# Kernel tuning notes

Hardware: AMD Instinct MI355X
Metric: run time of the kernel (lower is better)

The kernel has to match this reference:

```python
import jax, jax.numpy as jnp
import numpy as np

# Model hyperparameters (from init_kwargs)
D_MODEL = 1536
NUM_HEADS = 16
QUERY_GROUPS = 4
HEAD_DIM = D_MODEL // NUM_HEADS          # 96
HEADS_PER_GROUP = NUM_HEADS // QUERY_GROUPS
ROPE_THETA = 10000.0
T_GRID, H_GRID, W_GRID = 32, 16, 16      # patch_size
AXIS_DIM = HEAD_DIM // 3                 # 32 dims per RoPE axis (t, h, w)

B = 2
S = H_GRID * W_GRID                      # 256 spatial patches per frame
N = T_GRID * S


def _angles(pos, dim, theta):
    # pos: [P] int -> angles [P, dim//2]
    inv_freq = 1.0 / (theta ** (jnp.arange(0, dim, 2, dtype=jnp.float32) / dim))
    return pos.astype(jnp.float32)[:, None] * inv_freq[None, :]


def _rotate_half(x, cos, sin):
    # x: [..., d], cos/sin broadcastable to [..., d//2]; half-split rotation
    x1, x2 = jnp.split(x, 2, axis=-1)
    return jnp.concatenate([x1 * cos - x2 * sin, x2 * cos + x1 * sin], axis=-1)


def _rope3d(x, cos_t, sin_t, cos_h, sin_h, cos_w, sin_w):
    # x: [B, T, S, heads, HEAD_DIM]; apply RoPE per axis chunk (t | h | w)
    xt = _rotate_half(x[..., 0 * AXIS_DIM:1 * AXIS_DIM], cos_t, sin_t)
    xh = _rotate_half(x[..., 1 * AXIS_DIM:2 * AXIS_DIM], cos_h, sin_h)
    xw = _rotate_half(x[..., 2 * AXIS_DIM:3 * AXIS_DIM], cos_w, sin_w)
    return jnp.concatenate([xt, xh, xw], axis=-1)


def _rope_tables(T, S, dtype):
    ang_t = _angles(jnp.arange(T), AXIS_DIM, ROPE_THETA)            # [T, 16]
    pos_hw = jnp.arange(S)
    ang_h = _angles(pos_hw // W_GRID, AXIS_DIM, ROPE_THETA)          # [S, 16]
    ang_w = _angles(pos_hw % W_GRID, AXIS_DIM, ROPE_THETA)           # [S, 16]
    # broadcast shapes: t varies over frame axis, h/w over spatial axis
    cos_t = jnp.cos(ang_t).astype(dtype)[None, :, None, None, :]
    sin_t = jnp.sin(ang_t).astype(dtype)[None, :, None, None, :]
    cos_h = jnp.cos(ang_h).astype(dtype)[None, None, :, None, :]
    sin_h = jnp.sin(ang_h).astype(dtype)[None, None, :, None, :]
    cos_w = jnp.cos(ang_w).astype(dtype)[None, None, :, None, :]
    sin_w = jnp.sin(ang_w).astype(dtype)[None, None, :, None, :]
    return cos_t, sin_t, cos_h, sin_h, cos_w, sin_w


def setup_inputs() -> dict:
    key = jax.random.key(0)
    k1, k2, k3 = jax.random.split(key, 3)
    x = jax.random.normal(k1, (B, T_GRID, S, D_MODEL), dtype=jnp.float32)
    padding_mask = jnp.ones((B, N), dtype=bool)
    scale = D_MODEL ** -0.5
    qkv_out = (NUM_HEADS + 2 * QUERY_GROUPS) * HEAD_DIM  # 2304
    w_qkv = jax.random.normal(k2, (qkv_out, D_MODEL), dtype=jnp.float32) * scale
    w_o = jax.random.normal(k3, (D_MODEL, D_MODEL), dtype=jnp.float32) * scale
    return {"x": x, "padding_mask": padding_mask, "w_qkv": w_qkv, "w_o": w_o}


def reference(x, padding_mask, w_qkv, w_o):
    # Spatial attention mode (GQA SDPA fallback path, non-causal, key padding mask).
    Bx, T, Sx, D = x.shape
    qkv = jnp.einsum('btsd,ed->btse', x, w_qkv)  # fused qkv projection, no bias
    q_end = NUM_HEADS * HEAD_DIM
    k_end = q_end + QUERY_GROUPS * HEAD_DIM
    q = qkv[..., :q_end].reshape(Bx, T, Sx, NUM_HEADS, HEAD_DIM)
    k = qkv[..., q_end:k_end].reshape(Bx, T, Sx, QUERY_GROUPS, HEAD_DIM)
    v = qkv[..., k_end:].reshape(Bx, T, Sx, QUERY_GROUPS, HEAD_DIM)

    tabs = _rope_tables(T, Sx, x.dtype)
    q = _rope3d(q, *tabs)
    k = _rope3d(k, *tabs)

    # GQA: expand kv groups to num_heads
    k = jnp.repeat(k, HEADS_PER_GROUP, axis=3)
    v = jnp.repeat(v, HEADS_PER_GROUP, axis=3)

    # Spatial attention: each (b, t) frame attends over its S patches
    scale = 1.0 / np.sqrt(HEAD_DIM)
    scores = jnp.einsum('btqhd,btkhd->bthqk', q, k) * scale  # [B,T,H,S,S]
    key_mask = padding_mask.reshape(Bx, T, Sx)
    scores = jnp.where(key_mask[:, :, None, None, :], scores, jnp.asarray(-1e9, scores.dtype))
    attn = jax.nn.softmax(scores, axis=-1)
    out = jnp.einsum('bthqk,btkhd->btqhd', attn, v).reshape(Bx, T, Sx, D)
    return jnp.einsum('btsd,ed->btse', out, w_o)  # output projection
```

## Files before the change

### kernel.cpp

```cpp
#include <hip/hip_runtime.h>

typedef __bf16 bf16;
typedef __bf16 bf16x8 __attribute__((ext_vector_type(8)));
typedef float f32x4 __attribute__((ext_vector_type(4)));

#define AS1 __attribute__((address_space(1)))
#define AS3 __attribute__((address_space(3)))

__device__ __forceinline__ void gl_lds16(const bf16* g, bf16* s) {
  __builtin_amdgcn_global_load_lds((const AS1 void*)g, (AS3 void*)s, 16, 0, 0);
}

__global__ void cvt_f32_bf16(const float* __restrict__ in, bf16* __restrict__ out, long n) {
  long i = ((long)blockIdx.x * blockDim.x + threadIdx.x) * 8;
  if (i + 8 <= n) {
    float4 a = *(const float4*)(in + i);
    float4 b = *(const float4*)(in + i + 4);
    bf16x8 v;
    v[0] = (bf16)a.x; v[1] = (bf16)a.y; v[2] = (bf16)a.z; v[3] = (bf16)a.w;
    v[4] = (bf16)b.x; v[5] = (bf16)b.y; v[6] = (bf16)b.z; v[7] = (bf16)b.w;
    *(bf16x8*)(out + i) = v;
  }
}

__global__ void gemm_qkv(const bf16* __restrict__ A, const bf16* __restrict__ B,
                         bf16* __restrict__ C, bf16* __restrict__ Vt) {
  const int K = 1536;
  __shared__ __align__(16) bf16 As[128 * 32];
  __shared__ __align__(16) bf16 Bs[128 * 32];
  const int tid = threadIdx.x;
  const int wave = tid >> 6, lane = tid & 63;
  const int l16 = lane & 15, krow = lane >> 4;
  const int wm = (wave >> 1) * 64, wn = (wave & 1) * 64;
  const int bm = blockIdx.x, bn = blockIdx.y;
  const bf16* a_base = A + (long)bm * 128 * K;
  const bf16* b_base = B + (long)bn * 128 * K;

  f32x4 acc[4][4];
#pragma unroll
  for (int i = 0; i < 4; ++i)
#pragma unroll
    for (int j = 0; j < 4; ++j) {
      f32x4 z = {0.f, 0.f, 0.f, 0.f};
      acc[i][j] = z;
    }

  const int c0 = tid, c1 = 256 + tid;
  const int r0row = c0 >> 2, r0k = (c0 & 3) * 8;
  const int r1row = c1 >> 2, r1k = (c1 & 3) * 8;
  bf16* As_d0 = As + (wave * 64) * 8;
  bf16* As_d1 = As + (256 + wave * 64) * 8;
  bf16* Bs_d0 = Bs + (wave * 64) * 8;
  bf16* Bs_d1 = Bs + (256 + wave * 64) * 8;

  for (int k0 = 0; k0 < K; k0 += 32) {
    gl_lds16(a_base + (long)r0row * K + k0 + r0k, As_d0);
    gl_lds16(a_base + (long)r1row * K + k0 + r1k, As_d1);
    gl_lds16(b_base + (long)r0row * K + k0 + r0k, Bs_d0);
    gl_lds16(b_base + (long)r1row * K + k0 + r1k, Bs_d1);
    __syncthreads();
    bf16x8 af[4], bfr[4];
#pragma unroll
    for (int i = 0; i < 4; ++i)
      af[i] = *(const bf16x8*)(As + (wm + i * 16 + l16) * 32 + krow * 8);
#pragma unroll
    for (int j = 0; j < 4; ++j)
      bfr[j] = *(const bf16x8*)(Bs + (wn + j * 16 + l16) * 32 + krow * 8);
#pragma unroll
    for (int i = 0; i < 4; ++i)
#pragma unroll
      for (int j = 0; j < 4; ++j)
        acc[i][j] = __builtin_amdgcn_mfma_f32_16x16x32_bf16(af[i], bfr[j], acc[i][j], 0, 0, 0);
    __syncthreads();
  }

  const int row0 = bm * 128 + wm + krow * 4;
  const int col0 = bn * 128 + wn + l16;
  if (bn < 15) {
    const float invf = __powf(10000.f, -(float)l16 * (1.f / 16.f));
#pragma unroll
    for (int jp = 0; jp < 2; ++jp) {
      const int j0 = jp * 2;
      const int chunkbase = bn * 128 + wn + j0 * 16;
      const int rel = (chunkbase < 1536) ? chunkbase : chunkbase - 1536;
      const int ax = (rel % 96) / 32;
#pragma unroll
      for (int i = 0; i < 4; ++i)
#pragma unroll
        for (int r = 0; r < 4; ++r) {
          const int row = row0 + i * 16 + r;
          const int s = row & 255, t = (row >> 8) & 31;
          const int pos = (ax == 0) ? t : ((ax == 1) ? (s >> 4) : (s & 15));
          float c, sn;
          __sincosf((float)pos * invf, &sn, &c);
          const float x1 = acc[i][j0][r], x2 = acc[i][j0 + 1][r];
          C[(long)row * 2304 + col0 + j0 * 16] = (bf16)(x1 * c - x2 * sn);
          C[(long)row * 2304 + col0 + (j0 + 1) * 16] = (bf16)(x2 * c + x1 * sn);
        }
    }
  } else {
    const long bt = bm >> 1;
#pragma unroll
    for (int j = 0; j < 4; ++j) {
      const int rel = bn * 128 + wn + j * 16 - 1920;
      const int g = rel / 96;
      const int d = rel - g * 96 + l16;
      bf16* vdst = Vt + ((bt * 4 + g) * 96 + d) * 256;
#pragma unroll
      for (int i = 0; i < 4; ++i)
#pragma unroll
        for (int r = 0; r < 4; ++r) {
          const int row = row0 + i * 16 + r;
          vdst[row & 255] = (bf16)acc[i][j][r];
        }
    }
  }
}

template <typename CT>
__global__ void gemm_bt(const bf16* __restrict__ A, const bf16* __restrict__ B,
                        CT* __restrict__ C, int M, int N, int K) {
  __shared__ __align__(16) bf16 As[128 * 32];
  __shared__ __align__(16) bf16 Bs[128 * 32];
  const int tid = threadIdx.x;
  const int wave = tid >> 6, lane = tid & 63;
  const int l16 = lane & 15, krow = lane >> 4;
  const int wm = (wave >> 1) * 64, wn = (wave & 1) * 64;
  const long bm = blockIdx.x, bn = blockIdx.y;
  const bf16* a_base = A + bm * 128 * (long)K;
  const bf16* b_base = B + bn * 128 * (long)K;

  f32x4 acc[4][4];
#pragma unroll
  for (int i = 0; i < 4; ++i)
#pragma unroll
    for (int j = 0; j < 4; ++j) {
      f32x4 z = {0.f, 0.f, 0.f, 0.f};
      acc[i][j] = z;
    }

  const int c0 = tid, c1 = 256 + tid;
  const int r0row = c0 >> 2, r0k = (c0 & 3) * 8;
  const int r1row = c1 >> 2, r1k = (c1 & 3) * 8;
  bf16* As_d0 = As + (wave * 64) * 8;
  bf16* As_d1 = As + (256 + wave * 64) * 8;
  bf16* Bs_d0 = Bs + (wave * 64) * 8;
  bf16* Bs_d1 = Bs + (256 + wave * 64) * 8;

  for (int k0 = 0; k0 < K; k0 += 32) {
    gl_lds16(a_base + (long)r0row * K + k0 + r0k, As_d0);
    gl_lds16(a_base + (long)r1row * K + k0 + r1k, As_d1);
    gl_lds16(b_base + (long)r0row * K + k0 + r0k, Bs_d0);
    gl_lds16(b_base + (long)r1row * K + k0 + r1k, Bs_d1);
    __syncthreads();
    bf16x8 af[4], bfr[4];
#pragma unroll
    for (int i = 0; i < 4; ++i)
      af[i] = *(const bf16x8*)(As + (wm + i * 16 + l16) * 32 + krow * 8);
#pragma unroll
    for (int j = 0; j < 4; ++j)
      bfr[j] = *(const bf16x8*)(Bs + (wn + j * 16 + l16) * 32 + krow * 8);
#pragma unroll
    for (int i = 0; i < 4; ++i)
#pragma unroll
      for (int j = 0; j < 4; ++j)
        acc[i][j] = __builtin_amdgcn_mfma_f32_16x16x32_bf16(af[i], bfr[j], acc[i][j], 0, 0, 0);
    __syncthreads();
  }

  const long row0 = bm * 128 + wm + krow * 4;
  const long col0 = bn * 128 + wn + l16;
#pragma unroll
  for (int i = 0; i < 4; ++i)
#pragma unroll
    for (int j = 0; j < 4; ++j)
#pragma unroll
      for (int r = 0; r < 4; ++r)
        C[(row0 + i * 16 + r) * N + col0 + j * 16] = (CT)acc[i][j][r];
}

__global__ __launch_bounds__(256, 1) void attn(const bf16* __restrict__ qkv,
                                               const bf16* __restrict__ Vt,
                                               bf16* __restrict__ O) {
  extern __shared__ __align__(16) char smem[];
  bf16* Ks = (bf16*)smem;
  bf16* Pbase = (bf16*)(smem + 256 * 104 * 2);
  const int tid = threadIdx.x, wave = tid >> 6, lane = tid & 63;
  const int l16 = lane & 15, krow = lane >> 4;
  const int g = blockIdx.x;
  const long bt = blockIdx.y;
  const int h = g * 4 + wave;

  const bf16* kbase = qkv + bt * 256 * 2304 + 1536 + g * 96;
#pragma unroll
  for (int r = 0; r < 12; ++r) {
    int c = r * 256 + tid;
    int row = c / 12, part = c % 12;
    bf16x8 v = *(const bf16x8*)(kbase + (long)row * 2304 + part * 8);
    *(bf16x8*)(Ks + row * 104 + part * 8) = v;
  }

  const bf16* vt = Vt + (bt * 4 + g) * 96 * 256;
  bf16x8 vf[8][6];
#pragma unroll
  for (int ks = 0; ks < 8; ++ks)
#pragma unroll
    for (int j = 0; j < 6; ++j)
      vf[ks][j] = *(const bf16x8*)(vt + (j * 16 + l16) * 256 + ks * 32 + krow * 8);

  __syncthreads();

  bf16* Ps = Pbase + wave * (16 * 264);
  const bf16* qbase = qkv + bt * 256 * 2304 + h * 96;
  const float scale = 0.10206207261596575f;

  bf16x8 af[3], afn[3];
#pragma unroll
  for (int kk = 0; kk < 3; ++kk)
    af[kk] = *(const bf16x8*)(qbase + (long)l16 * 2304 + kk * 32 + krow * 8);

  for (int ch = 0; ch < 16; ++ch) {
    if (ch < 15) {
#pragma unroll
      for (int kk = 0; kk < 3; ++kk)
        afn[kk] = *(const bf16x8*)(qbase + (long)((ch + 1) * 16 + l16) * 2304 + kk * 32 + krow * 8);
    }

    f32x4 sacc[16];
#pragma unroll
    for (int j = 0; j < 16; ++j) {
      f32x4 z = {0.f, 0.f, 0.f, 0.f};
      sacc[j] = z;
    }
#pragma unroll
    for (int j = 0; j < 16; ++j)
#pragma unroll
      for (int kk = 0; kk < 3; ++kk) {
        bf16x8 bfj = *(const bf16x8*)(Ks + (j * 16 + l16) * 104 + kk * 32 + krow * 8);
        sacc[j] = __builtin_amdgcn_mfma_f32_16x16x32_bf16(af[kk], bfj, sacc[j], 0, 0, 0);
      }

    float mx[4], sm[4];
#pragma unroll
    for (int r = 0; r < 4; ++r) { mx[r] = -3.0e38f; sm[r] = 0.f; }
#pragma unroll
    for (int j = 0; j < 16; ++j)
#pragma unroll
      for (int r = 0; r < 4; ++r) mx[r] = fmaxf(mx[r], sacc[j][r]);
#pragma unroll
    for (int m = 8; m >= 1; m >>= 1)
#pragma unroll
      for (int r = 0; r < 4; ++r) mx[r] = fmaxf(mx[r], __shfl_xor(mx[r], m, 64));
#pragma unroll
    for (int j = 0; j < 16; ++j)
#pragma unroll
      for (int r = 0; r < 4; ++r) {
        float e = __expf((sacc[j][r] - mx[r]) * scale);
        sacc[j][r] = e;
        sm[r] += e;
      }
#pragma unroll
    for (int m = 8; m >= 1; m >>= 1)
#pragma unroll
      for (int r = 0; r < 4; ++r) sm[r] += __shfl_xor(sm[r], m, 64);
    float rcpv[4];
#pragma unroll
    for (int r = 0; r < 4; ++r) rcpv[r] = 1.f / sm[r];

#pragma unroll
    for (int j = 0; j < 16; ++j)
#pragma unroll
      for (int r = 0; r < 4; ++r)
        Ps[(krow * 4 + r) * 264 + j * 16 + l16] = (bf16)(sacc[j][r] * rcpv[r]);

    f32x4 oacc[6];
#pragma unroll
    for (int j = 0; j < 6; ++j) {
      f32x4 z = {0.f, 0.f, 0.f, 0.f};
      oacc[j] = z;
    }
#pragma unroll
    for (int ks = 0; ks < 8; ++ks) {
      bf16x8 a = *(const bf16x8*)(Ps + l16 * 264 + ks * 32 + krow * 8);
#pragma unroll
      for (int j = 0; j < 6; ++j)
        oacc[j] = __builtin_amdgcn_mfma_f32_16x16x32_bf16(a, vf[ks][j], oacc[j], 0, 0, 0);
    }
    const long orow = bt * 256 + ch * 16 + krow * 4;
#pragma unroll
    for (int j = 0; j < 6; ++j)
#pragma unroll
      for (int r = 0; r < 4; ++r)
        O[(orow + r) * 1536 + h * 96 + j * 16 + l16] = (bf16)oacc[j][r];

#pragma unroll
    for (int kk = 0; kk < 3; ++kk) af[kk] = afn[kk];
  }
}

extern "C" void kernel_launch(void* const* d_in, const int* in_sizes, int n_in,
                              void* d_out, int out_size, void* d_ws, size_t ws_size,
                              hipStream_t stream) {
  const float* x = (const float*)d_in[0];
  const float* wqkv = (const float*)d_in[2];
  const float* wo = (const float*)d_in[3];
  float* out = (float*)d_out;

  char* ws = (char*)d_ws;
  const long NX = 16384L * 1536;
  const long NWQ = 2304L * 1536;
  const long NWO = 1536L * 1536;
  bf16* xb = (bf16*)ws;
  bf16* qkv = (bf16*)(ws + 50331648L);
  bf16* vt = (bf16*)(ws + 50331648L + 75497472L);
  bf16* wqb = (bf16*)(ws + 138412032L);
  bf16* wob = (bf16*)(ws + 145489920L);

  cvt_f32_bf16<<<(int)(NX / 8 / 256), 256, 0, stream>>>(x, xb, NX);
  cvt_f32_bf16<<<(int)(NWQ / 8 / 256), 256, 0, stream>>>(wqkv, wqb, NWQ);
  cvt_f32_bf16<<<(int)(NWO / 8 / 256), 256, 0, stream>>>(wo, wob, NWO);

  gemm_qkv<<<dim3(128, 18), 256, 0, stream>>>(xb, wqb, qkv, vt);

  bf16* O = xb;
  const int attn_lds = 256 * 104 * 2 + 4 * 16 * 264 * 2;
  attn<<<dim3(4, 64), 256, attn_lds, stream>>>(qkv, vt, O);

  gemm_bt<float><<<dim3(128, 12), 256, 0, stream>>>(O, wob, out, 16384, 1536, 1536);
}
```

Before: 526.9 us.

## Replace 128x128 GEMMs with pipelined 256x256 double-buffered swizzled GEMM kernel

Both the QKV projection and the output projection now use a new 256x256-tile GEMM with 8 waves, BK=64 and double-buffered LDS. The K-loop is split into four sub-phases that interleave global-to-LDS prefetch with MFMA work, using raw barriers, waitcnt and setprio. An XOR swizzle on LDS rows is meant to avoid bank conflicts. The aim is more data reuse per tile and hiding load latency behind compute, at the cost of 128KB LDS per block and fewer blocks (576 and 384) to fill the device.

```diff
diff --git a/kernel.cpp b/kernel.cpp
--- a/kernel.cpp
+++ b/kernel.cpp
@@ -10,6 +10,10 @@
 __device__ __forceinline__ void gl_lds16(const bf16* g, bf16* s) {
   __builtin_amdgcn_global_load_lds((const AS1 void*)g, (AS3 void*)s, 16, 0, 0);
 }
+
+#define FENCE() asm volatile("" ::: "memory")
+#define BARRIER() __builtin_amdgcn_s_barrier()
+#define LGKM0() asm volatile("s_waitcnt lgkmcnt(0)" ::: "memory")
 
 __global__ void cvt_f32_bf16(const float* __restrict__ in, bf16* __restrict__ out, long n) {
   long i = ((long)blockIdx.x * blockDim.x + threadIdx.x) * 8;
@@ -23,160 +27,202 @@
   }
 }
 
-__global__ void gemm_qkv(const bf16* __restrict__ A, const bf16* __restrict__ B,
-                         bf16* __restrict__ C, bf16* __restrict__ Vt) {
-  const int K = 1536;
-  __shared__ __align__(16) bf16 As[128 * 32];
-  __shared__ __align__(16) bf16 Bs[128 * 32];
+__device__ __forceinline__ void stage_half(const bf16* __restrict__ gsrc, int ldk,
+                                           bf16* ldst, int tid) {
+#pragma unroll
+  for (int q = 0; q < 2; ++q) {
+    const int idx = q * 512 + tid;
+    const int r = idx >> 3;
+    const int c = tid & 7;
+    const bf16* src = gsrc + (long)r * ldk + ((c ^ (r & 7)) << 3);
+    bf16* dst = ldst + q * 4096 + (tid >> 6) * 512;
+    gl_lds16(src, dst);
+  }
+}
+
+template <int EPI, typename CT>
+__global__ __launch_bounds__(512, 2) void gemm256(const bf16* __restrict__ A,
+                                                  const bf16* __restrict__ B,
+                                                  CT* __restrict__ C,
+                                                  bf16* __restrict__ Vt) {
+  constexpr int K = 1536;
+  constexpr int NT = K / 64;
+  extern __shared__ __align__(16) char smem[];
+  bf16* const Ab0 = (bf16*)smem;
+  bf16* const Ab1 = Ab0 + 16384;
+  bf16* const Bb0 = Ab1 + 16384;
+  bf16* const Bb1 = Bb0 + 16384;
+
   const int tid = threadIdx.x;
   const int wave = tid >> 6, lane = tid & 63;
   const int l16 = lane & 15, krow = lane >> 4;
-  const int wm = (wave >> 1) * 64, wn = (wave & 1) * 64;
-  const int bm = blockIdx.x, bn = blockIdx.y;
-  const bf16* a_base = A + (long)bm * 128 * K;
-  const bf16* b_base = B + (long)bn * 128 * K;
-
-  f32x4 acc[4][4];
-#pragma unroll
-  for (int i = 0; i < 4; ++i)
+  const int wr = wave >> 2, wc = wave & 3;
+  const long bm = blockIdx.x, bn = blockIdx.y;
+
+  const bf16* a_base = A + bm * 256 * K;
+  const bf16* b_base = B + bn * 256 * K;
+
+  stage_half(a_base, K, Ab0, tid);
+  stage_half(a_base + 128L * K, K, Ab0 + 8192, tid);
+  stage_half(b_base, K, Bb0, tid);
+  stage_half(b_base + 128L * K, K, Bb0 + 8192, tid);
+  stage_half(a_base + 64, K, Ab1, tid);
+
+  f32x4 acc[8][4];
+#pragma unroll
+  for (int a = 0; a < 8; ++a)
 #pragma unroll
     for (int j = 0; j < 4; ++j) {
       f32x4 z = {0.f, 0.f, 0.f, 0.f};
-      acc[i][j] = z;
-    }
-
-  const int c0 = tid, c1 = 256 + tid;
-  const int r0row = c0 >> 2, r0k = (c0 & 3) * 8;
-  const int r1row = c1 >> 2, r1k = (c1 & 3) * 8;
-  bf16* As_d0 = As + (wave * 64) * 8;
-  bf16* As_d1 = As + (256 + wave * 64) * 8;
-  bf16* Bs_d0 = Bs + (wave * 64) * 8;
-  bf16* Bs_d1 = Bs + (256 + wave * 64) * 8;
-
-  for (int k0 = 0; k0 < K; k0 += 32) {
-    gl_lds16(a_base + (long)r0row * K + k0 + r0k, As_d0);
-    gl_lds16(a_base + (long)r1row * K + k0 + r1k, As_d1);
-    gl_lds16(b_base + (long)r0row * K + k0 + r0k, Bs_d0);
-    gl_lds16(b_base + (long)r1row * K + k0 + r1k, Bs_d1);
-    __syncthreads();
-    bf16x8 af[4], bfr[4];
+      acc[a][j] = z;
+    }
+
+  asm volatile("s_waitcnt vmcnt(2)" ::: "memory");
+  BARRIER();
+  FENCE();
+
+  bf16* Acur = Ab0; bf16* Anxt = Ab1;
+  bf16* Bcur = Bb0; bf16* Bnxt = Bb1;
+
+  const int swz = l16 & 7;
+
+#pragma unroll 1
+  for (int t = 0; t < NT; ++t) {
+    bf16x8 Af[4], Bf0[4], Bf1[4];
+
+#pragma unroll
+    for (int i = 0; i < 4; ++i) {
+      const int r = i * 32 + wr * 16 + l16;
+      Af[i] = *(const bf16x8*)(Acur + r * 64 + ((krow ^ swz) << 3));
+    }
+#pragma unroll
+    for (int j = 0; j < 4; ++j) {
+      const int r = (wc & 1) * 64 + j * 16 + l16;
+      Bf0[j] = *(const bf16x8*)(Bcur + (wc >> 1) * 8192 + r * 64 + ((krow ^ swz) << 3));
+    }
+    if (t + 1 < NT) stage_half(a_base + 128L * K + (t + 1) * 64, K, Anxt + 8192, tid);
+    FENCE(); BARRIER(); LGKM0();
+    __builtin_amdgcn_s_setprio(1);
 #pragma unroll
     for (int i = 0; i < 4; ++i)
-      af[i] = *(const bf16x8*)(As + (wm + i * 16 + l16) * 32 + krow * 8);
-#pragma unroll
-    for (int j = 0; j < 4; ++j)
-      bfr[j] = *(const bf16x8*)(Bs + (wn + j * 16 + l16) * 32 + krow * 8);
+#pragma unroll
+      for (int j = 0; j < 4; ++j)
+        acc[i][j] = __builtin_amdgcn_mfma_f32_16x16x32_bf16(Af[i], Bf0[j], acc[i][j], 0, 0, 0);
+    __builtin_amdgcn_s_setprio(0);
+    FENCE(); BARRIER(); FENCE();
+
+#pragma unroll
+    for (int i = 0; i < 4; ++i) {
+      const int r = i * 32 + wr * 16 + l16;
+      Af[i] = *(const bf16x8*)(Acur + r * 64 + (((krow + 4) ^ swz) << 3));
+    }
+#pragma unroll
+    for (int j = 0; j < 4; ++j) {
+      const int r = (wc & 1) * 64 + j * 16 + l16;
+      Bf1[j] = *(const bf16x8*)(Bcur + (wc >> 1) * 8192 + r * 64 + (((krow + 4) ^ swz) << 3));
+    }
+    if (t + 1 < NT) stage_half(b_base + (t + 1) * 64, K, Bnxt, tid);
+    FENCE(); BARRIER(); LGKM0();
+    __builtin_amdgcn_s_setprio(1);
 #pragma unroll
     for (int i = 0; i < 4; ++i)
 #pragma unroll
       for (int j = 0; j < 4; ++j)
-        acc[i][j] = __builtin_amdgcn_mfma_f32_16x16x32_bf16(af[i], bfr[j], acc[i][j], 0, 0, 0);
-    __syncthreads();
-  }
-
-  const int row0 = bm * 128 + wm + krow * 4;
-  const int col0 = bn * 128 + wn + l16;
-  if (bn < 15) {
-    const float invf = __powf(10000.f, -(float)l16 * (1.f / 16.f));
-#pragma unroll
-    for (int jp = 0; jp < 2; ++jp) {
-      const int j0 = jp * 2;
-      const int chunkbase = bn * 128 + wn + j0 * 16;
-      const int rel = (chunkbase < 1536) ? chunkbase : chunkbase - 1536;
-      const int ax = (rel % 96) / 32;
-#pragma unroll
-      for (int i = 0; i < 4; ++i)
-#pragma unroll
-        for (int r = 0; r < 4; ++r) {
-          const int row = row0 + i * 16 + r;
-          const int s = row & 255, t = (row >> 8) & 31;
-          const int pos = (ax == 0) ? t : ((ax == 1) ? (s >> 4) : (s & 15));
-          float c, sn;
-          __sincosf((float)pos * invf, &sn, &c);
-          const float x1 = acc[i][j0][r], x2 = acc[i][j0 + 1][r];
-          C[(long)row * 2304 + col0 + j0 * 16] = (bf16)(x1 * c - x2 * sn);
-          C[(long)row * 2304 + col0 + (j0 + 1) * 16] = (bf16)(x2 * c + x1 * sn);
+        acc[i][j] = __builtin_amdgcn_mfma_f32_16x16x32_bf16(Af[i], Bf1[j], acc[i][j], 0, 0, 0);
+    __builtin_amdgcn_s_setprio(0);
+    FENCE(); BARRIER(); FENCE();
+
+#pragma unroll
+    for (int i = 0; i < 4; ++i) {
+      const int r = i * 32 + wr * 16 + l16;
+      Af[i] = *(const bf16x8*)(Acur + 8192 + r * 64 + ((krow ^ swz) << 3));
+    }
+    if (t + 1 < NT) stage_half(b_base + 128L * K + (t + 1) * 64, K, Bnxt + 8192, tid);
+    FENCE(); BARRIER(); LGKM0();
+    __builtin_amdgcn_s_setprio(1);
+#pragma unroll
+    for (int i = 0; i < 4; ++i)
+#pragma unroll
+      for (int j = 0; j < 4; ++j)
+        acc[4 + i][j] = __builtin_amdgcn_mfma_f32_16x16x32_bf16(Af[i], Bf0[j], acc[4 + i][j], 0, 0, 0);
+    __builtin_amdgcn_s_setprio(0);
+    FENCE(); BARRIER(); FENCE();
+
+#pragma unroll
+    for (int i = 0; i < 4; ++i) {
+      const int r = i * 32 + wr * 16 + l16;
+      Af[i] = *(const bf16x8*)(Acur + 8192 + r * 64 + (((krow + 4) ^ swz) << 3));
+    }
+    if (t + 2 < NT) stage_half(a_base + (t + 2) * 64, K, Acur, tid);
+    FENCE(); BARRIER(); LGKM0();
+    __builtin_amdgcn_s_setprio(1);
+#pragma unroll
+    for (int i = 0; i < 4; ++i)
+#pragma unroll
+      for (int j = 0; j < 4; ++j)
+        acc[4 + i][j] = __builtin_amdgcn_mfma_f32_16x16x32_bf16(Af[i], Bf1[j], acc[4 + i][j], 0, 0, 0);
+    __builtin_amdgcn_s_setprio(0);
+    FENCE();
+    if (t + 2 < NT) { asm volatile("s_waitcnt vmcnt(2)" ::: "memory"); }
+    else            { asm volatile("s_waitcnt vmcnt(0)" ::: "memory"); }
+    BARRIER(); FENCE();
+
+    bf16* tp = Acur; Acur = Anxt; Anxt = tp;
+    tp = Bcur; Bcur = Bnxt; Bnxt = tp;
+  }
+
+  const int colbase = (int)bn * 256 + wc * 64;
+  if constexpr (EPI == 0) {
+    if (colbase < 1920) {
+      const float invf = __powf(10000.f, -(float)l16 * (1.f / 16.f));
+#pragma unroll
+      for (int jp = 0; jp < 2; ++jp) {
+        const int chunkbase = colbase + jp * 32;
+        const int rel = (chunkbase < 1536) ? chunkbase : chunkbase - 1536;
+        const int ax = (rel % 96) / 32;
+#pragma unroll
+        for (int a = 0; a < 8; ++a) {
+          const long rowb = bm * 256 + ((a >> 2) * 8 + (a & 3) * 2 + wr) * 16 + krow * 4;
+#pragma unroll
+          for (int r = 0; r < 4; ++r) {
+            const long row = rowb + r;
+            const int s = (int)(row & 255), tt = (int)((row >> 8) & 31);
+            const int pos = (ax == 0) ? tt : ((ax == 1) ? (s >> 4) : (s & 15));
+            float cv, sv;
+            __sincosf((float)pos * invf, &sv, &cv);
+            const float x1 = acc[a][jp * 2][r], x2 = acc[a][jp * 2 + 1][r];
+            C[row * 2304 + colbase + jp * 32 + l16] = (CT)(x1 * cv - x2 * sv);
+            C[row * 2304 + colbase + jp * 32 + 16 + l16] = (CT)(x2 * cv + x1 * sv);
+          }
         }
+      }
+    } else {
+#pragma unroll
+      for (int j = 0; j < 4; ++j) {
+        const int rel = colbase + j * 16 - 1920;
+        const int g = rel / 96;
+        const int d = rel - g * 96 + l16;
+        bf16* vdst = Vt + ((bm * 4 + g) * 96 + d) * 256;
+#pragma unroll
+        for (int a = 0; a < 8; ++a) {
+          const long rowb = bm * 256 + ((a >> 2) * 8 + (a & 3) * 2 + wr) * 16 + krow * 4;
+#pragma unroll
+          for (int r = 0; r < 4; ++r)
+            vdst[(rowb + r) & 255] = (bf16)acc[a][j][r];
+        }
+      }
     }
   } else {
-    const long bt = bm >> 1;
-#pragma unroll
-    for (int j = 0; j < 4; ++j) {
-      const int rel = bn * 128 + wn + j * 16 - 1920;
-      const int g = rel / 96;
-      const int d = rel - g * 96 + l16;
-      bf16* vdst = Vt + ((bt * 4 + g) * 96 + d) * 256;
-#pragma unroll
-      for (int i = 0; i < 4; ++i)
-#pragma unroll
-        for (int r = 0; r < 4; ++r) {
-          const int row = row0 + i * 16 + r;
-          vdst[row & 255] = (bf16)acc[i][j][r];
-        }
-    }
-  }
-}
-
-template <typename CT>
-__global__ void gemm_bt(const bf16* __restrict__ A, const bf16* __restrict__ B,
-                        CT* __restrict__ C, int M, int N, int K) {
-  __shared__ __align__(16) bf16 As[128 * 32];
-  __shared__ __align__(16) bf16 Bs[128 * 32];
-  const int tid = threadIdx.x;
-  const int wave = tid >> 6, lane = tid & 63;
-  const int l16 = lane & 15, krow = lane >> 4;
-  const int wm = (wave >> 1) * 64, wn = (wave & 1) * 64;
-  const long bm = blockIdx.x, bn = blockIdx.y;
-  const bf16* a_base = A + bm * 128 * (long)K;
-  const bf16* b_base = B + bn * 128 * (long)K;
-
-  f32x4 acc[4][4];
-#pragma unroll
-  for (int i = 0; i < 4; ++i)
-#pragma unroll
-    for (int j = 0; j < 4; ++j) {
-      f32x4 z = {0.f, 0.f, 0.f, 0.f};
-      acc[i][j] = z;
-    }
-
-  const int c0 = tid, c1 = 256 + tid;
-  const int r0row = c0 >> 2, r0k = (c0 & 3) * 8;
-  const int r1row = c1 >> 2, r1k = (c1 & 3) * 8;
-  bf16* As_d0 = As + (wave * 64) * 8;
-  bf16* As_d1 = As + (256 + wave * 64) * 8;
-  bf16* Bs_d0 = Bs + (wave * 64) * 8;
-  bf16* Bs_d1 = Bs + (256 + wave * 64) * 8;
-
-  for (int k0 = 0; k0 < K; k0 += 32) {
-    gl_lds16(a_base + (long)r0row * K + k0 + r0k, As_d0);
-    gl_lds16(a_base + (long)r1row * K + k0 + r1k, As_d1);
-    gl_lds16(b_base + (long)r0row * K + k0 + r0k, Bs_d0);
-    gl_lds16(b_base + (long)r1row * K + k0 + r1k, Bs_d1);
-    __syncthreads();
-    bf16x8 af[4], bfr[4];
-#pragma unroll
-    for (int i = 0; i < 4; ++i)
-      af[i] = *(const bf16x8*)(As + (wm + i * 16 + l16) * 32 + krow * 8);
-#pragma unroll
-    for (int j = 0; j < 4; ++j)
-      bfr[j] = *(const bf16x8*)(Bs + (wn + j * 16 + l16) * 32 + krow * 8);
-#pragma unroll
-    for (int i = 0; i < 4; ++i)
-#pragma unroll
-      for (int j = 0; j < 4; ++j)
-        acc[i][j] = __builtin_amdgcn_mfma_f32_16x16x32_bf16(af[i], bfr[j], acc[i][j], 0, 0, 0);
-    __syncthreads();
-  }
-
-  const long row0 = bm * 128 + wm + krow * 4;
-  const long col0 = bn * 128 + wn + l16;
-#pragma unroll
-  for (int i = 0; i < 4; ++i)
-#pragma unroll
-    for (int j = 0; j < 4; ++j)
-#pragma unroll
-      for (int r = 0; r < 4; ++r)
-        C[(row0 + i * 16 + r) * N + col0 + j * 16] = (CT)acc[i][j][r];
+#pragma unroll
+    for (int a = 0; a < 8; ++a) {
+      const long rowb = bm * 256 + ((a >> 2) * 8 + (a & 3) * 2 + wr) * 16 + krow * 4;
+#pragma unroll
+      for (int j = 0; j < 4; ++j)
+#pragma unroll
+        for (int r = 0; r < 4; ++r)
+          C[(rowb + r) * 1536 + colbase + j * 16 + l16] = (CT)acc[a][j][r];
+    }
+  }
 }
 
 __global__ __launch_bounds__(256, 1) void attn(const bf16* __restrict__ qkv,
@@ -320,11 +366,11 @@
   cvt_f32_bf16<<<(int)(NWQ / 8 / 256), 256, 0, stream>>>(wqkv, wqb, NWQ);
   cvt_f32_bf16<<<(int)(NWO / 8 / 256), 256, 0, stream>>>(wo, wob, NWO);
 
-  gemm_qkv<<<dim3(128, 18), 256, 0, stream>>>(xb, wqb, qkv, vt);
+  gemm256<0, bf16><<<dim3(64, 9), 512, 131072, stream>>>(xb, wqb, qkv, vt);
 
   bf16* O = xb;
   const int attn_lds = 256 * 104 * 2 + 4 * 16 * 264 * 2;
   attn<<<dim3(4, 64), 256, attn_lds, stream>>>(qkv, vt, O);
 
-  gemm_bt<float><<<dim3(128, 12), 256, 0, stream>>>(O, wob, out, 16384, 1536, 1536);
-}
+  gemm256<1, float><<<dim3(64, 6), 512, 131072, stream>>>(O, wob, out, nullptr);
+}
```

Result: faster. 510.2 us (-3.2%).

## Replace GEMM kernels with triple-buffered 128x256 swizzled-LDS pipelined GEMM

Applied to the files above, without the earlier changes.

Both projection GEMMs now share one kernel with 512 threads, a 128x256 tile, and a three-stage LDS ring. Global-to-LDS loads for tile k+2 are issued while MFMAs run on tile k, with explicit vmcnt waits and barriers. The LDS layout uses an XOR swizzle to avoid bank conflicts, and MFMA sections get raised wave priority. The goal is to hide global memory latency and cut the two __syncthreads per 32-wide K step, at the cost of more LDS per block and trickier synchronisation.

```diff
diff --git a/kernel.cpp b/kernel.cpp
--- a/kernel.cpp
+++ b/kernel.cpp
@@ -10,6 +10,10 @@
 __device__ __forceinline__ void gl_lds16(const bf16* g, bf16* s) {
   __builtin_amdgcn_global_load_lds((const AS1 void*)g, (AS3 void*)s, 16, 0, 0);
 }
+
+#define FENCE() asm volatile("" ::: "memory")
+#define BARRIER() __builtin_amdgcn_s_barrier()
+#define LGKM0() asm volatile("s_waitcnt lgkmcnt(0)" ::: "memory")
 
 __global__ void cvt_f32_bf16(const float* __restrict__ in, bf16* __restrict__ out, long n) {
   long i = ((long)blockIdx.x * blockDim.x + threadIdx.x) * 8;
@@ -23,18 +27,41 @@
   }
 }
 
-__global__ void gemm_qkv(const bf16* __restrict__ A, const bf16* __restrict__ B,
-                         bf16* __restrict__ C, bf16* __restrict__ Vt) {
-  const int K = 1536;
-  __shared__ __align__(16) bf16 As[128 * 32];
-  __shared__ __align__(16) bf16 Bs[128 * 32];
+template <int ROWS>
+__device__ __forceinline__ void stage32(const bf16* __restrict__ g, int ldk,
+                                        bf16* slab, int tid) {
+  const int r_lo = tid >> 2;
+  const int csw = ((tid & 3) ^ (((tid >> 2) & 3) ^ ((tid >> 4) & 3))) << 3;
+  bf16* dst = slab + (tid >> 6) * 512;
+#pragma unroll
+  for (int q = 0; q < ROWS / 128; ++q)
+    gl_lds16(g + (long)(q * 128 + r_lo) * ldk + csw, dst + q * 4096);
+}
+
+template <int EPI, typename CT>
+__global__ __launch_bounds__(512, 4) void gemm128(const bf16* __restrict__ A,
+                                                  const bf16* __restrict__ B,
+                                                  CT* __restrict__ C,
+                                                  bf16* __restrict__ Vt) {
+  constexpr int K = 1536;
+  constexpr int NT = K / 32;
+  extern __shared__ __align__(16) char smem[];
+  bf16* const As = (bf16*)smem;
+  bf16* const Bs = As + 3 * 4096;
+
   const int tid = threadIdx.x;
   const int wave = tid >> 6, lane = tid & 63;
   const int l16 = lane & 15, krow = lane >> 4;
-  const int wm = (wave >> 1) * 64, wn = (wave & 1) * 64;
-  const int bm = blockIdx.x, bn = blockIdx.y;
-  const bf16* a_base = A + (long)bm * 128 * K;
-  const bf16* b_base = B + (long)bn * 128 * K;
+  const int wr = wave >> 2, wc = wave & 3;
+  const long bm = blockIdx.x, bn = blockIdx.y;
+
+  const bf16* a_base = A + bm * 128 * K;
+  const bf16* b_base = B + bn * 256 * K;
+
+  const int rs = (l16 & 3) ^ ((l16 >> 2) & 3);
+  const int koff = ((krow ^ rs) << 3);
+  const int aoff = (wr * 64 + l16) * 32 + koff;
+  const int boff = (wc * 64 + l16) * 32 + koff;
 
   f32x4 acc[4][4];
 #pragma unroll
@@ -45,138 +72,98 @@
       acc[i][j] = z;
     }
 
-  const int c0 = tid, c1 = 256 + tid;
-  const int r0row = c0 >> 2, r0k = (c0 & 3) * 8;
-  const int r1row = c1 >> 2, r1k = (c1 & 3) * 8;
-  bf16* As_d0 = As + (wave * 64) * 8;
-  bf16* As_d1 = As + (256 + wave * 64) * 8;
-  bf16* Bs_d0 = Bs + (wave * 64) * 8;
-  bf16* Bs_d1 = Bs + (256 + wave * 64) * 8;
-
-  for (int k0 = 0; k0 < K; k0 += 32) {
-    gl_lds16(a_base + (long)r0row * K + k0 + r0k, As_d0);
-    gl_lds16(a_base + (long)r1row * K + k0 + r1k, As_d1);
-    gl_lds16(b_base + (long)r0row * K + k0 + r0k, Bs_d0);
-    gl_lds16(b_base + (long)r1row * K + k0 + r1k, Bs_d1);
-    __syncthreads();
-    bf16x8 af[4], bfr[4];
+  stage32<128>(a_base, K, As, tid);
+  stage32<256>(b_base, K, Bs, tid);
+  stage32<128>(a_base + 32, K, As + 4096, tid);
+  stage32<256>(b_base + 32, K, Bs + 8192, tid);
+  asm volatile("s_waitcnt vmcnt(3)" ::: "memory");
+  BARRIER();
+  FENCE();
+
+#define PHASE(T, CUR, PRE)                                                          \
+  {                                                                                 \
+    bf16x8 Af[4], Bf[4];                                                            \
+    _Pragma("unroll") for (int i = 0; i < 4; ++i)                                   \
+        Af[i] = *(const bf16x8*)(As + (CUR) * 4096 + aoff + i * 512);               \
+    _Pragma("unroll") for (int j = 0; j < 4; ++j)                                   \
+        Bf[j] = *(const bf16x8*)(Bs + (CUR) * 8192 + boff + j * 512);               \
+    if ((T) + 2 < NT) {                                                             \
+      stage32<128>(a_base + ((T) + 2) * 32, K, As + (PRE) * 4096, tid);             \
+      stage32<256>(b_base + ((T) + 2) * 32, K, Bs + (PRE) * 8192, tid);             \
+    }                                                                               \
+    FENCE(); BARRIER(); LGKM0();                                                    \
+    __builtin_amdgcn_s_setprio(1);                                                  \
+    _Pragma("unroll") for (int i = 0; i < 4; ++i)                                   \
+        _Pragma("unroll") for (int j = 0; j < 4; ++j)                               \
+            acc[i][j] =                                                             \
+                __builtin_amdgcn_mfma_f32_16x16x32_bf16(Af[i], Bf[j], acc[i][j],    \
+                                                        0, 0, 0);                   \
+    __builtin_amdgcn_s_setprio(0);                                                  \
+    FENCE();                                                                        \
+    if ((T) + 2 < NT) { asm volatile("s_waitcnt vmcnt(3)" ::: "memory"); }          \
+    else              { asm volatile("s_waitcnt vmcnt(0)" ::: "memory"); }          \
+    BARRIER(); FENCE();                                                             \
+  }
+
+#pragma unroll 1
+  for (int tt = 0; tt < NT; tt += 3) {
+    PHASE(tt, 0, 2);
+    PHASE(tt + 1, 1, 0);
+    PHASE(tt + 2, 2, 1);
+  }
+#undef PHASE
+
+  const int colbase = (int)bn * 256 + wc * 64;
+  if constexpr (EPI == 0) {
+    if (colbase < 1920) {
+      const float invf = __powf(10000.f, -(float)l16 * (1.f / 16.f));
+#pragma unroll
+      for (int jp = 0; jp < 2; ++jp) {
+        const int chunkbase = colbase + jp * 32;
+        const int rel = (chunkbase < 1536) ? chunkbase : chunkbase - 1536;
+        const int ax = (rel % 96) / 32;
+#pragma unroll
+        for (int i = 0; i < 4; ++i)
+#pragma unroll
+          for (int r = 0; r < 4; ++r) {
+            const long row = bm * 128 + wr * 64 + i * 16 + krow * 4 + r;
+            const int sp = (int)(row & 255), tfr = (int)((row >> 8) & 31);
+            const int pos = (ax == 0) ? tfr : ((ax == 1) ? (sp >> 4) : (sp & 15));
+            float cv, sv;
+            __sincosf((float)pos * invf, &sv, &cv);
+            const float x1 = acc[i][jp * 2][r], x2 = acc[i][jp * 2 + 1][r];
+            C[row * 2304 + chunkbase + l16] = (CT)(x1 * cv - x2 * sv);
+            C[row * 2304 + chunkbase + 16 + l16] = (CT)(x2 * cv + x1 * sv);
+          }
+      }
+    } else {
+      const long bt = bm >> 1;
+#pragma unroll
+      for (int j = 0; j < 4; ++j) {
+        const int rel = colbase + j * 16 - 1920;
+        const int g = rel / 96;
+        const int d = rel - g * 96 + l16;
+        bf16* vdst = Vt + ((bt * 4 + g) * 96 + d) * 256;
+#pragma unroll
+        for (int i = 0; i < 4; ++i)
+#pragma unroll
+          for (int r = 0; r < 4; ++r) {
+            const long row = bm * 128 + wr * 64 + i * 16 + krow * 4 + r;
+            vdst[row & 255] = (bf16)acc[i][j][r];
+          }
+      }
+    }
+  } else {
 #pragma unroll
     for (int i = 0; i < 4; ++i)
-      af[i] = *(const bf16x8*)(As + (wm + i * 16 + l16) * 32 + krow * 8);
-#pragma unroll
-    for (int j = 0; j < 4; ++j)
-      bfr[j] = *(const bf16x8*)(Bs + (wn + j * 16 + l16) * 32 + krow * 8);
-#pragma unroll
-    for (int i = 0; i < 4; ++i)
-#pragma unroll
-      for (int j = 0; j < 4; ++j)
-        acc[i][j] = __builtin_amdgcn_mfma_f32_16x16x32_bf16(af[i], bfr[j], acc[i][j], 0, 0, 0);
-    __syncthreads();
-  }
-
-  const int row0 = bm * 128 + wm + krow * 4;
-  const int col0 = bn * 128 + wn + l16;
-  if (bn < 15) {
-    const float invf = __powf(10000.f, -(float)l16 * (1.f / 16.f));
-#pragma unroll
-    for (int jp = 0; jp < 2; ++jp) {
-      const int j0 = jp * 2;
-      const int chunkbase = bn * 128 + wn + j0 * 16;
-      const int rel = (chunkbase < 1536) ? chunkbase : chunkbase - 1536;
-      const int ax = (rel % 96) / 32;
-#pragma unroll
-      for (int i = 0; i < 4; ++i)
-#pragma unroll
-        for (int r = 0; r < 4; ++r) {
-          const int row = row0 + i * 16 + r;
-          const int s = row & 255, t = (row >> 8) & 31;
-          const int pos = (ax == 0) ? t : ((ax == 1) ? (s >> 4) : (s & 15));
-          float c, sn;
-          __sincosf((float)pos * invf, &sn, &c);
-          const float x1 = acc[i][j0][r], x2 = acc[i][j0 + 1][r];
-          C[(long)row * 2304 + col0 + j0 * 16] = (bf16)(x1 * c - x2 * sn);
-          C[(long)row * 2304 + col0 + (j0 + 1) * 16] = (bf16)(x2 * c + x1 * sn);
-        }
-    }
-  } else {
-    const long bt = bm >> 1;
-#pragma unroll
-    for (int j = 0; j < 4; ++j) {
-      const int rel = bn * 128 + wn + j * 16 - 1920;
-      const int g = rel / 96;
-      const int d = rel - g * 96 + l16;
-      bf16* vdst = Vt + ((bt * 4 + g) * 96 + d) * 256;
-#pragma unroll
-      for (int i = 0; i < 4; ++i)
-#pragma unroll
-        for (int r = 0; r < 4; ++r) {
-          const int row = row0 + i * 16 + r;
-          vdst[row & 255] = (bf16)acc[i][j][r];
-        }
-    }
-  }
-}
-
-template <typename CT>
-__global__ void gemm_bt(const bf16* __restrict__ A, const bf16* __restrict__ B,
-                        CT* __restrict__ C, int M, int N, int K) {
-  __shared__ __align__(16) bf16 As[128 * 32];
-  __shared__ __align__(16) bf16 Bs[128 * 32];
-  const int tid = threadIdx.x;
-  const int wave = tid >> 6, lane = tid & 63;
-  const int l16 = lane & 15, krow = lane >> 4;
-  const int wm = (wave >> 1) * 64, wn = (wave & 1) * 64;
-  const long bm = blockIdx.x, bn = blockIdx.y;
-  const bf16* a_base = A + bm * 128 * (long)K;
-  const bf16* b_base = B + bn * 128 * (long)K;
-
-  f32x4 acc[4][4];
-#pragma unroll
-  for (int i = 0; i < 4; ++i)
-#pragma unroll
-    for (int j = 0; j < 4; ++j) {
-      f32x4 z = {0.f, 0.f, 0.f, 0.f};
-      acc[i][j] = z;
-    }
-
-  const int c0 = tid, c1 = 256 + tid;
-  const int r0row = c0 >> 2, r0k = (c0 & 3) * 8;
-  const int r1row = c1 >> 2, r1k = (c1 & 3) * 8;
-  bf16* As_d0 = As + (wave * 64) * 8;
-  bf16* As_d1 = As + (256 + wave * 64) * 8;
-  bf16* Bs_d0 = Bs + (wave * 64) * 8;
-  bf16* Bs_d1 = Bs + (256 + wave * 64) * 8;
-
-  for (int k0 = 0; k0 < K; k0 += 32) {
-    gl_lds16(a_base + (long)r0row * K + k0 + r0k, As_d0);
-    gl_lds16(a_base + (long)r1row * K + k0 + r1k, As_d1);
-    gl_lds16(b_base + (long)r0row * K + k0 + r0k, Bs_d0);
-    gl_lds16(b_base + (long)r1row * K + k0 + r1k, Bs_d1);
-    __syncthreads();
-    bf16x8 af[4], bfr[4];
-#pragma unroll
-    for (int i = 0; i < 4; ++i)
-      af[i] = *(const bf16x8*)(As + (wm + i * 16 + l16) * 32 + krow * 8);
-#pragma unroll
-    for (int j = 0; j < 4; ++j)
-      bfr[j] = *(const bf16x8*)(Bs + (wn + j * 16 + l16) * 32 + krow * 8);
-#pragma unroll
-    for (int i = 0; i < 4; ++i)
-#pragma unroll
-      for (int j = 0; j < 4; ++j)
-        acc[i][j] = __builtin_amdgcn_mfma_f32_16x16x32_bf16(af[i], bfr[j], acc[i][j], 0, 0, 0);
-    __syncthreads();
-  }
-
-  const long row0 = bm * 128 + wm + krow * 4;
-  const long col0 = bn * 128 + wn + l16;
-#pragma unroll
-  for (int i = 0; i < 4; ++i)
-#pragma unroll
-    for (int j = 0; j < 4; ++j)
-#pragma unroll
-      for (int r = 0; r < 4; ++r)
-        C[(row0 + i * 16 + r) * N + col0 + j * 16] = (CT)acc[i][j][r];
+#pragma unroll
+      for (int r = 0; r < 4; ++r) {
+        const long row = bm * 128 + wr * 64 + i * 16 + krow * 4 + r;
+#pragma unroll
+        for (int j = 0; j < 4; ++j)
+          C[row * 1536 + colbase + j * 16 + l16] = (CT)acc[i][j][r];
+      }
+  }
 }
 
 __global__ __launch_bounds__(256, 1) void attn(const bf16* __restrict__ qkv,
@@ -320,11 +307,13 @@
   cvt_f32_bf16<<<(int)(NWQ / 8 / 256), 256, 0, stream>>>(wqkv, wqb, NWQ);
   cvt_f32_bf16<<<(int)(NWO / 8 / 256), 256, 0, stream>>>(wo, wob, NWO);
 
-  gemm_qkv<<<dim3(128, 18), 256, 0, stream>>>(xb, wqb, qkv, vt);
+  const int gemm_lds = 3 * (4096 + 8192) * 2;
+
+  gemm128<0, bf16><<<dim3(128, 9), 512, gemm_lds, stream>>>(xb, wqb, qkv, vt);
 
   bf16* O = xb;
   const int attn_lds = 256 * 104 * 2 + 4 * 16 * 264 * 2;
   attn<<<dim3(4, 64), 256, attn_lds, stream>>>(qkv, vt, O);
 
-  gemm_bt<float><<<dim3(128, 12), 256, 0, stream>>>(O, wob, out, 16384, 1536, 1536);
-}
+  gemm128<1, float><<<dim3(128, 6), 512, gemm_lds, stream>>>(O, wob, out, nullptr);
+}
```

New measurement: 626.7 us. 18.9% more time.
